# Performance work log

Hardware: AMD Instinct MI355X
Metric: run time of the kernel (lower is better)

The kernel has to match this reference:

```python
import jax, jax.numpy as jnp
import numpy as np

EPS = 1e-7
INF = 1e8
SOFT_CENTER_RADIUS = 3.0
TOPK = 13
IOU_WEIGHT = 3.0
NUM_CLASSES = 80
N_PRIORS = 33600
NUM_GT = 256
IMG = 1024.0


def setup_inputs() -> dict:
    key = jax.random.key(0)
    k1, k2, k3, k4, k5, k6, k7 = jax.random.split(key, 7)
    n, g, c = N_PRIORS, NUM_GT, NUM_CLASSES
    pred_scores = jax.random.normal(k1, (n, c), jnp.float32)
    # priors: (cx, cy, stride, stride)
    ctr = jax.random.uniform(k2, (n, 2), jnp.float32) * IMG
    stride = jnp.full((n, 1), 8.0, jnp.float32)
    priors = jnp.concatenate([ctr, stride, stride], axis=-1)
    # predicted boxes, x1y1x2y2
    pwh = jax.random.uniform(k3, (n, 2), jnp.float32) * 96.0 + 8.0
    pctr = jax.random.uniform(k4, (n, 2), jnp.float32) * IMG
    pred_bboxes = jnp.concatenate([pctr - pwh / 2, pctr + pwh / 2], axis=-1)
    # gt boxes, x1y1x2y2
    gwh = jax.random.uniform(k5, (g, 2), jnp.float32) * 192.0 + 16.0
    gctr = jax.random.uniform(k6, (g, 2), jnp.float32) * IMG
    gt_bboxes = jnp.concatenate([gctr - gwh / 2, gctr + gwh / 2], axis=-1)
    gt_labels = jax.random.randint(k7, (g,), 0, c, dtype=jnp.int32).astype(jnp.int64)
    return {"pred_scores": pred_scores, "priors": priors,
            "pred_bboxes": pred_bboxes, "gt_bboxes": gt_bboxes,
            "gt_labels": gt_labels}


def _pairwise_iou(a, b):
    # a: (n,4), b: (g,4), x1y1x2y2 -> (n,g)
    area_a = (a[:, 2] - a[:, 0]) * (a[:, 3] - a[:, 1])
    area_b = (b[:, 2] - b[:, 0]) * (b[:, 3] - b[:, 1])
    lt = jnp.maximum(a[:, None, :2], b[None, :, :2])
    rb = jnp.minimum(a[:, None, 2:], b[None, :, 2:])
    wh = jnp.clip(rb - lt, 0.0, None)
    inter = wh[..., 0] * wh[..., 1]
    union = area_a[:, None] + area_b[None, :] - inter
    return inter / jnp.maximum(union, 1e-6)


def reference(pred_scores, priors, pred_bboxes, gt_bboxes, gt_labels):
    n, g = pred_bboxes.shape[0], gt_bboxes.shape[0]
    gt_labels = gt_labels.astype(jnp.int32)

    # ---- find_inside_points (box_dim == 4) ----
    pts = priors[:, :2]                                   # (n,2)
    lt = pts[:, None, :] - gt_bboxes[None, :, :2]
    rb = gt_bboxes[None, :, 2:] - pts[:, None, :]
    is_in_gts = jnp.min(jnp.concatenate([lt, rb], -1), -1) > 0   # (n,g)
    pad_bbox_flag = gt_bboxes.sum(-1) > 0                        # (g,)
    is_in_gts = is_in_gts & pad_bbox_flag[None, :]
    valid_mask = jnp.any(is_in_gts, -1)                          # (n,)

    # ---- soft center prior ----
    gt_center = (gt_bboxes[:, :2] + gt_bboxes[:, 2:]) * 0.5      # (g,2)
    dist = jnp.sqrt(((pts[:, None, :] - gt_center[None, :, :]) ** 2).sum(-1))
    dist = dist / priors[:, 2:3]                                 # / stride
    dist = dist * valid_mask[:, None].astype(dist.dtype)
    soft_center_prior = jnp.power(10.0, dist - SOFT_CENTER_RADIUS)

    # ---- iou cost ----
    ious = _pairwise_iou(pred_bboxes, gt_bboxes)                 # (n,g)
    iou_cost = -jnp.log(ious + EPS) * IOU_WEIGHT

    # ---- soft classification cost (BCE-with-logits, iou targets) ----
    logits = pred_scores[:, gt_labels]                           # (n,g)
    scale = jnp.abs(ious - jax.nn.sigmoid(logits)) ** 2
    bce = jnp.maximum(logits, 0) - logits * ious + jnp.log1p(jnp.exp(-jnp.abs(logits)))
    cost = bce * scale + iou_cost + soft_center_prior
    cost = jnp.where(valid_mask[:, None], cost, INF)

    # ---- dynamic k matching (vectorized over GTs) ----
    K = min(TOPK, n)
    topk_ious, _ = jax.lax.top_k(ious.T, K)                      # (g,K)
    dynamic_ks = jnp.clip(topk_ious.sum(-1).astype(jnp.int32), 1, None)  # (g,)
    _, cand_idx = jax.lax.top_k(-cost.T, K)                      # (g,K) lowest-cost priors per gt
    sel = (jnp.arange(K)[None, :] < dynamic_ks[:, None]).astype(jnp.float32)
    matching = jnp.zeros((g, n), jnp.float32).at[
        jnp.arange(g)[:, None], cand_idx].set(sel).T             # (n,g)

    # resolve priors matched to multiple gts -> keep min-cost gt
    multi = matching.sum(-1) > 1
    onehot_min = jax.nn.one_hot(jnp.argmin(cost, -1), g, dtype=jnp.float32)
    matching = jnp.where(multi[:, None], onehot_min, matching)

    fg = matching.sum(-1) > 0
    matched_gt_inds = jnp.argmax(matching, -1)                   # (n,)
    matched_pred_ious = (matching * ious).sum(-1)                # (n,)

    final = fg & valid_mask
    assigned_gt_inds = jnp.where(final, matched_gt_inds + 1, 0)
    assigned_labels = jnp.where(final, gt_labels[matched_gt_inds], -1)
    max_overlaps = jnp.where(final, matched_pred_ious, -INF)
    return assigned_gt_inds, max_overlaps, assigned_labels
```

## Files before the change

### kernel.cpp

```cpp
#include <hip/hip_runtime.h>
#include <cstdint>

#define NPRI 33600
#define NGT  256
#define NCLS 80
#define KTOP 13
#define INF_F 1.0e8f
#define EPS_F 1e-7f
#define L10 3.3219280948873623f
#define SCN_T 1024
#define NW   (SCN_T / 64)
#define CAPI 4096
#define CAPC 1024
#define RFIX 5.5f
#define NPAD (4 * SCN_T)
#define PREP_BLKS ((NPRI + 255) / 256)
#define NEGINF __int_as_float(0xff800000)

typedef unsigned long long u64;

__device__ __forceinline__ int get_label(const void* p, int j, int is64) {
    if (is64) return (int)((const long long*)p)[j];
    return ((const int*)p)[j];
}

__device__ __forceinline__ float wave_max_bc_f32(float v) {
    #pragma unroll
    for (int off = 32; off > 0; off >>= 1) v = fmaxf(v, __shfl_down(v, off, 64));
    return __int_as_float(__builtin_amdgcn_readfirstlane(__float_as_int(v)));
}
__device__ __forceinline__ u64 wave_min_bc_u64(u64 v) {
    #pragma unroll
    for (int off = 32; off > 0; off >>= 1) { u64 o = __shfl_down(v, off, 64); v = (o < v) ? o : v; }
    unsigned lo = (unsigned)__builtin_amdgcn_readfirstlane((int)(v & 0xffffffffull));
    unsigned hi = (unsigned)__builtin_amdgcn_readfirstlane((int)(v >> 32));
    return (((u64)hi) << 32) | lo;
}
template<int NSL>
__device__ __forceinline__ void wave_merge_max13_f32(float (&l)[NSL], float* dst, int lane) {
    int p = 0;
    for (int r = 0; r < KTOP; ++r) {
        float cur = NEGINF;
        #pragma unroll
        for (int s = 0; s < NSL; ++s) if (s == p) cur = l[NSL - 1 - s];
        float bm = wave_max_bc_f32(cur);
        u64 m = __ballot(cur == bm && bm != NEGINF);
        int first = __ffsll(m) - 1;
        if (lane == first) p++;
        if (lane == 0) dst[r] = bm;
    }
}
template<int NSL>
__device__ __forceinline__ void wave_merge_minN(u64 (&l)[NSL], u64* dst, int lane) {
    int p = 0;
    for (int r = 0; r < KTOP; ++r) {
        u64 cur = ~0ull;
        #pragma unroll
        for (int s = 0; s < NSL; ++s) if (s == p) cur = l[s];
        u64 bm = wave_min_bc_u64(cur);
        if (cur == bm && bm != ~0ull) p++;
        if (lane == 0) dst[r] = bm;
    }
}

__device__ __forceinline__ float iou_exact(float4 pb, float areap, float gx1, float gy1,
                                           float gx2, float gy2, float areag) {
    float iw = fmaxf(fminf(pb.z, gx2) - fmaxf(pb.x, gx1), 0.0f);
    float ih = fmaxf(fminf(pb.w, gy2) - fmaxf(pb.y, gy1), 0.0f);
    float inter = iw * ih;
    return inter / fmaxf(areap + areag - inter, 1e-6f);
}
__device__ __forceinline__ float cost_exact(float4 p2, float gcx, float gcy,
                                            float l, float iou) {
    float dx = p2.x - gcx, dy = p2.y - gcy;
    float dist = sqrtf(dx * dx + dy * dy) / p2.z;
    float soft = exp2f((dist - 3.0f) * L10);
    float sig = 1.0f / (1.0f + expf(-l));
    float dd = iou - sig;
    float bce = fmaxf(l, 0.0f) - l * iou + log1pf(expf(-fabsf(l)));
    float iouc = -logf(iou + EPS_F) * 3.0f;
    return bce * (dd * dd) + iouc + soft;
}

__global__ __launch_bounds__(256) void k_prep(
        const float* __restrict__ priors, const float* __restrict__ gt,
        const void* labels, const float* __restrict__ pboxes,
        float4* __restrict__ pbp,
        int* count, int* firstgt, int* flag) {
    __shared__ float4 gbox[NGT];
    __shared__ int    gpad[NGT];
    __shared__ int    bad;
    const int tid = threadIdx.x;
    const int b = blockIdx.x;
    if (b == 0 && tid == 0) bad = 0;
    {
        float4 bx = ((const float4*)gt)[tid];
        gbox[tid] = bx;
        gpad[tid] = ((bx.x + bx.y + bx.z + bx.w) > 0.0f) ? 1 : 0;
    }
    __syncthreads();
    if (b == 0 && tid < 128) {
        long long v = ((const long long*)labels)[tid];
        if (v < 0 || v >= NCLS) atomicOr(&bad, 1);
    }
    int g = b * 256 + tid;
    if (g < NPAD) {
        pbp[2 * (NPRI + g)]     = make_float4(0.f, 0.f, 0.f, 0.f);
        pbp[2 * (NPRI + g) + 1] = make_float4(0.f, 0.f, 1.f, -1.0f);
    }
    if (g < NPRI) {
        count[g] = 0; firstgt[g] = NGT;
        float4 pr = ((const float4*)priors)[g];
        float px = pr.x, py = pr.y;
        int v = 0;
        for (int j = 0; j < NGT; ++j) {
            float4 bx = gbox[j];
            float m = fminf(fminf(px - bx.x, py - bx.y), fminf(bx.z - px, bx.w - py));
            if (m > 0.0f && gpad[j]) { v = 1; break; }
        }
        float rad = pr.z * RFIX;
        float w = v ? rad * rad * (1.0f + 1e-5f) : -1.0f;
        pbp[2 * g]     = ((const float4*)pboxes)[g];
        pbp[2 * g + 1] = make_float4(px, py, pr.z, w);
    }
    if (b == 0) {
        __syncthreads();
        if (tid == 0) *flag = bad ? 0 : 1;
    }
}

#define STEPM(K, PB, P2) { \
    const int i = i0 + (it + K) * SCN_T; \
    float4 pbc = PB; float4 p2c = P2; \
    const int ip = i + 4 * SCN_T; \
    PB = pbp[2 * ip]; \
    P2 = pbp[2 * ip + 1]; \
    float areap = (pbc.z - pbc.x) * (pbc.w - pbc.y); \
    float iw = fmaxf(fminf(pbc.z, gx2) - fmaxf(pbc.x, gx1), 0.0f); \
    float ih = fmaxf(fminf(pbc.w, gy2) - fmaxf(pbc.y, gy1), 0.0f); \
    float inter = iw * ih; \
    float iou = inter / fmaxf(areap + areag - inter, 1e-6f); \
    if (iou > 0.0f) { \
        int p = atomicAdd(&s_ni, 1); \
        if (p < CAPI) liou[p] = iou; \
    } \
    float dx = p2c.x - gcx, dy = p2c.y - gcy; \
    if (dx * dx + dy * dy <= p2c.w) { \
        int p = atomicAdd(&s_nc, 1); \
        if (p < CAPC) lcost[p] = i; \
    } \
}

__global__ __launch_bounds__(SCN_T) void k_scan(
        const float* __restrict__ scores,
        const float4* __restrict__ pbp,
        const float* __restrict__ gt, const void* labels, const int* flag,
        int* count, int* firstgt) {
    const int tid = threadIdx.x, lane = tid & 63, wid = tid >> 6;
    const int j = blockIdx.x;
    const int is64 = *flag;

    const float4 gb = ((const float4*)gt)[j];
    const float gx1 = gb.x, gy1 = gb.y, gx2 = gb.z, gy2 = gb.w;
    const float areag = (gx2 - gx1) * (gy2 - gy1);
    const float gcx = (gx1 + gx2) * 0.5f, gcy = (gy1 + gy2) * 0.5f;
    const int lab = get_label(labels, j, is64);

    __shared__ int s_ni, s_nc, s_mode;
    __shared__ float s_dmax;
    __shared__ float liou[CAPI];
    __shared__ int lcost[CAPC];
    __shared__ float wiof[(NW - 1) * KTOP];
    __shared__ u64 wco[NW * KTOP];
    __shared__ u64 csel[KTOP];
    __shared__ float s_iou13[KTOP];
    if (tid == 0) { s_ni = 0; s_nc = 0; }
    __syncthreads();

    {
        const int i0 = tid;
        float4 pb0 = pbp[2 * i0],               p20 = pbp[2 * i0 + 1];
        float4 pb1 = pbp[2 * (i0 + SCN_T)],     p21 = pbp[2 * (i0 + SCN_T) + 1];
        float4 pb2 = pbp[2 * (i0 + 2 * SCN_T)], p22 = pbp[2 * (i0 + 2 * SCN_T) + 1];
        float4 pb3 = pbp[2 * (i0 + 3 * SCN_T)], p23 = pbp[2 * (i0 + 3 * SCN_T) + 1];
        for (int it = 0; it < 32; it += 4) {
            STEPM(0, pb0, p20)
            STEPM(1, pb1, p21)
            STEPM(2, pb2, p22)
            STEPM(3, pb3, p23)
        }
        {
            const int i = i0 + 32 * SCN_T;
            if (i < NPRI) {
                float4 pbc = pb0; float4 p2c = p20;
                float areap = (pbc.z - pbc.x) * (pbc.w - pbc.y);
                float iw = fmaxf(fminf(pbc.z, gx2) - fmaxf(pbc.x, gx1), 0.0f);
                float ih = fmaxf(fminf(pbc.w, gy2) - fmaxf(pbc.y, gy1), 0.0f);
                float inter = iw * ih;
                float iou = inter / fmaxf(areap + areag - inter, 1e-6f);
                if (iou > 0.0f) {
                    int p = atomicAdd(&s_ni, 1);
                    if (p < CAPI) liou[p] = iou;
                }
                float dx = p2c.x - gcx, dy = p2c.y - gcy;
                if (dx * dx + dy * dy <= p2c.w) {
                    int p = atomicAdd(&s_nc, 1);
                    if (p < CAPC) lcost[p] = i;
                }
            }
        }
    }
    __syncthreads();
    const int ni = s_ni, nc = s_nc;
    const int ncc = (nc < CAPC) ? nc : CAPC;
    const bool fI = (ni > CAPI);

    if (wid == 0) {
        u64 lf[KTOP];
        #pragma unroll
        for (int s = 0; s < KTOP; ++s) lf[s] = ~0ull;
        for (int k = lane; k < ncc; k += 64) {
            int i = lcost[k];
            float4 pb = pbp[2 * i];
            float4 p2 = pbp[2 * i + 1];
            float areap = (pb.z - pb.x) * (pb.w - pb.y);
            float iou = iou_exact(pb, areap, gx1, gy1, gx2, gy2, areag);
            float ec = cost_exact(p2, gcx, gcy, scores[(size_t)i * NCLS + lab], iou);
            u64 ck = (((u64)__float_as_uint(ec)) << 32) | (unsigned)i;
            if (ck < lf[KTOP - 1]) {
                lf[KTOP - 1] = ck;
                #pragma unroll
                for (int s = KTOP - 1; s > 0; --s)
                    if (lf[s] < lf[s - 1]) { u64 t = lf[s]; lf[s] = lf[s - 1]; lf[s - 1] = t; }
            }
        }
        wave_merge_minN<KTOP>(lf, csel, lane);
        if (lane == 0) {
            u64 tk = csel[KTOP - 1];
            int mode; float dmax = 0.0f;
            if (tk == ~0ull) mode = 2;
            else {
                float tau = __uint_as_float((unsigned)(tk >> 32));
                if (!(tau < 9.0e7f)) mode = 2;
                else {
                    dmax = 3.0f + __log2f(tau + 1e-5f) * (1.0f / L10) + 4e-3f;
                    mode = (dmax > RFIX || nc > CAPC) ? 1 : 0;
                }
            }
            s_mode = mode; s_dmax = dmax;
        }
    } else if (!fI) {
        float lf[KTOP];
        #pragma unroll
        for (int s = 0; s < KTOP; ++s) lf[s] = NEGINF;
        int nn = (ni < CAPI) ? ni : CAPI;
        for (int k = (wid - 1) * 64 + lane; k < nn; k += 64 * (NW - 1)) {
            float v = liou[k];
            if (v > lf[0]) {
                lf[0] = v;
                #pragma unroll
                for (int s = 0; s < KTOP - 1; ++s)
                    if (lf[s] > lf[s + 1]) { float t = lf[s]; lf[s] = lf[s + 1]; lf[s + 1] = t; }
            }
        }
        wave_merge_max13_f32<KTOP>(lf, &wiof[(wid - 1) * KTOP], lane);
    }
    __syncthreads();

    if (fI) {
        if (wid > 0) {
            float lf[KTOP];
            #pragma unroll
            for (int s = 0; s < KTOP; ++s) lf[s] = NEGINF;
            for (int i = (wid - 1) * 64 + lane; i < NPRI; i += 64 * (NW - 1)) {
                float4 pb = pbp[2 * i];
                float areap = (pb.z - pb.x) * (pb.w - pb.y);
                float iou = iou_exact(pb, areap, gx1, gy1, gx2, gy2, areag);
                if (iou > 0.0f && iou > lf[0]) {
                    lf[0] = iou;
                    #pragma unroll
                    for (int s = 0; s < KTOP - 1; ++s)
                        if (lf[s] > lf[s + 1]) { float t = lf[s]; lf[s] = lf[s + 1]; lf[s + 1] = t; }
                }
            }
            wave_merge_max13_f32<KTOP>(lf, &wiof[(wid - 1) * KTOP], lane);
        }
        __syncthreads();
    }

    if (wid == 0) {
        int p = 0;
        for (int r = 0; r < KTOP; ++r) {
            float cur = (lane < NW - 1 && p < KTOP) ? wiof[lane * KTOP + p] : NEGINF;
            float bm = wave_max_bc_f32(cur);
            u64 m = __ballot(cur == bm && bm != NEGINF);
            int first = __ffsll(m) - 1;
            if (lane == first) p++;
            if (lane == 0) s_iou13[r] = bm;
        }
    }

    int mode = s_mode;
    if (mode == 1) {
        const float dmax = s_dmax;
        if (tid == 0) s_nc = 0;
        __syncthreads();
        for (int i = tid; i < NPRI; i += SCN_T) {
            float4 p2 = pbp[2 * i + 1];
            if (p2.w > 0.0f) {
                float dx = p2.x - gcx, dy = p2.y - gcy;
                float rad = p2.z * dmax;
                if (dx * dx + dy * dy <= rad * rad * (1.0f + 1e-5f)) {
                    int p = atomicAdd(&s_nc, 1);
                    if (p < CAPC) lcost[p] = i;
                }
            }
        }
        __syncthreads();
        int nc2 = s_nc;
        if (nc2 <= CAPC) {
            if (wid == 0) {
                u64 lf[KTOP];
                #pragma unroll
                for (int s = 0; s < KTOP; ++s) lf[s] = ~0ull;
                for (int k = lane; k < nc2; k += 64) {
                    int i = lcost[k];
                    float4 pb = pbp[2 * i];
                    float4 p2 = pbp[2 * i + 1];
                    float areap = (pb.z - pb.x) * (pb.w - pb.y);
                    float iou = iou_exact(pb, areap, gx1, gy1, gx2, gy2, areag);
                    float ec = cost_exact(p2, gcx, gcy, scores[(size_t)i * NCLS + lab], iou);
                    u64 ck = (((u64)__float_as_uint(ec)) << 32) | (unsigned)i;
                    if (ck < lf[KTOP - 1]) {
                        lf[KTOP - 1] = ck;
                        #pragma unroll
                        for (int s = KTOP - 1; s > 0; --s)
                            if (lf[s] < lf[s - 1]) { u64 t = lf[s]; lf[s] = lf[s - 1]; lf[s - 1] = t; }
                    }
                }
                wave_merge_minN<KTOP>(lf, csel, lane);
            }
        } else {
            mode = 2;
        }
        __syncthreads();
    }
    if (mode == 2) {
        u64 lf[KTOP];
        #pragma unroll
        for (int s = 0; s < KTOP; ++s) lf[s] = ~0ull;
        for (int i = tid; i < NPRI; i += SCN_T) {
            float4 pb = pbp[2 * i];
            float4 p2 = pbp[2 * i + 1];
            float areap = (pb.z - pb.x) * (pb.w - pb.y);
            float iou = iou_exact(pb, areap, gx1, gy1, gx2, gy2, areag);
            float ec = INF_F;
            if (p2.w > 0.0f) ec = cost_exact(p2, gcx, gcy, scores[(size_t)i * NCLS + lab], iou);
            u64 k2 = (((u64)__float_as_uint(ec)) << 32) | (unsigned)i;
            if (k2 < lf[KTOP - 1]) {
                lf[KTOP - 1] = k2;
                #pragma unroll
                for (int s = KTOP - 1; s > 0; --s)
                    if (lf[s] < lf[s - 1]) { u64 t = lf[s]; lf[s] = lf[s - 1]; lf[s - 1] = t; }
            }
        }
        wave_merge_minN<KTOP>(lf, &wco[wid * KTOP], lane);
        __syncthreads();
        if (wid == 0) {
            int p = 0;
            for (int r = 0; r < KTOP; ++r) {
                u64 cur = (lane < NW && p < KTOP) ? wco[lane * KTOP + p] : ~0ull;
                u64 bm = wave_min_bc_u64(cur);
                if (cur == bm && bm != ~0ull) p++;
                if (lane == 0) csel[r] = bm;
            }
        }
        __syncthreads();
    }

    __syncthreads();
    if (wid == 0) {
        float tsum = 0.0f;
        #pragma unroll
        for (int r = 0; r < KTOP; ++r) {
            float v = s_iou13[r];
            tsum += (v == NEGINF) ? 0.0f : v;
        }
        int ks = (int)tsum;
        if (ks < 1) ks = 1;
        if (lane < KTOP && lane < ks) {
            u64 mine = csel[lane];
            if (mine != ~0ull) {
                int idx = (int)(unsigned)(mine & 0xFFFFFFFFull);
                atomicAdd(&count[idx], 1);
                atomicMin(&firstgt[idx], j);
            }
        }
    }
}

__global__ __launch_bounds__(256) void k_assign(
        const float* __restrict__ scores,
        const float4* __restrict__ pbp, const float* __restrict__ gt,
        const void* labels, const int* flag,
        const int* __restrict__ count, const int* __restrict__ firstgt,
        float* __restrict__ out) {
    __shared__ float4 gbox[NGT];
    __shared__ int glab[NGT];
    __shared__ float gcxs[NGT], gcys[NGT], gareas[NGT];
    __shared__ int s_nm;
    __shared__ int s_mlist[256];
    __shared__ u64 red4[4];
    const int tid = threadIdx.x;
    const int is64 = *flag;
    {
        float4 b = ((const float4*)gt)[tid];
        gbox[tid] = b;
        glab[tid] = get_label(labels, tid, is64);
        gcxs[tid] = (b.x + b.z) * 0.5f;
        gcys[tid] = (b.y + b.w) * 0.5f;
        gareas[tid] = (b.z - b.x) * (b.w - b.y);
    }
    if (tid == 0) s_nm = 0;
    __syncthreads();
    const int i = blockIdx.x * 256 + tid;
    const bool act = (i < NPRI);
    if (act) {
        float4 p2 = pbp[2 * i + 1];
        int v = (p2.w > 0.0f) ? 1 : 0;
        int c = count[i];
        float o0 = 0.0f, o1 = -INF_F, o2 = -1.0f;
        if (v && c == 1) {
            int j = firstgt[i];
            float4 pb = pbp[2 * i];
            float areap = (pb.z - pb.x) * (pb.w - pb.y);
            float4 g = gbox[j];
            float iw = fmaxf(fminf(pb.z, g.z) - fmaxf(pb.x, g.x), 0.0f);
            float ih = fmaxf(fminf(pb.w, g.w) - fmaxf(pb.y, g.y), 0.0f);
            float inter = iw * ih;
            float iou = inter / fmaxf(areap + gareas[j] - inter, 1e-6f);
            o0 = (float)(j + 1); o1 = iou; o2 = (float)glab[j];
        } else if (v && c > 1) {
            int p = atomicAdd(&s_nm, 1);
            s_mlist[p] = i;
        }
        out[i] = o0;
        out[NPRI + i] = o1;
        out[2 * NPRI + i] = o2;
    }
    __syncthreads();
    const int nm = s_nm;
    const int j = tid;
    for (int m = 0; m < nm; ++m) {
        const int ii = s_mlist[m];
        float4 pb = pbp[2 * ii];
        float4 p2 = pbp[2 * ii + 1];
        float areap = (pb.z - pb.x) * (pb.w - pb.y);

        float4 g = gbox[j];
        float iw = fmaxf(fminf(pb.z, g.z) - fmaxf(pb.x, g.x), 0.0f);
        float ih = fmaxf(fminf(pb.w, g.w) - fmaxf(pb.y, g.y), 0.0f);
        float inter = iw * ih;
        float iou = inter / fmaxf(areap + gareas[j] - inter, 1e-6f);
        float dx = p2.x - gcxs[j], dy = p2.y - gcys[j];
        float dist = sqrtf(dx * dx + dy * dy) / p2.z;
        float soft = exp2f((dist - 3.0f) * L10);
        float l = scores[(size_t)ii * NCLS + glab[j]];
        float sig = 1.0f / (1.0f + expf(-l));
        float dd = iou - sig;
        float bce = fmaxf(l, 0.0f) - l * iou + log1pf(expf(-fabsf(l)));
        float cost = bce * (dd * dd) + (-logf(iou + EPS_F) * 3.0f) + soft;

        u64 key = (((u64)__float_as_uint(cost)) << 32) | (unsigned)j;
        u64 v = key;
        #pragma unroll
        for (int off = 32; off > 0; off >>= 1) {
            u64 o = __shfl_down(v, off, 64);
            v = (o < v) ? o : v;
        }
        if ((tid & 63) == 0) red4[tid >> 6] = v;
        __syncthreads();
        u64 best = red4[0];
        #pragma unroll
        for (int q = 1; q < 4; ++q) best = (red4[q] < best) ? red4[q] : best;
        if (key == best) {
            out[ii] = (float)(j + 1);
            out[NPRI + ii] = iou;
            out[2 * NPRI + ii] = (float)glab[j];
        }
        __syncthreads();
    }
}

extern "C" void kernel_launch(void* const* d_in, const int* in_sizes, int n_in,
                              void* d_out, int out_size, void* d_ws, size_t ws_size,
                              hipStream_t stream) {
    const float* scores = (const float*)d_in[0];
    const float* priors = (const float*)d_in[1];
    const float* pboxes = (const float*)d_in[2];
    const float* gt     = (const float*)d_in[3];
    const void*  labels = d_in[4];
    float* out = (float*)d_out;

    char* ws = (char*)d_ws;
    size_t off = 0;
    auto alloc = [&](size_t bytes) { size_t o = off; off = (off + bytes + 255) & ~(size_t)255; return o; };
    int*    flag     = (int*)(ws + alloc(4));
    int*    count    = (int*)(ws + alloc((size_t)NPRI * 4));
    int*    firstgt  = (int*)(ws + alloc((size_t)NPRI * 4));
    float4* pbp      = (float4*)(ws + alloc((size_t)(NPRI + NPAD) * 32));
    (void)ws_size;

    hipLaunchKernelGGL(k_prep, dim3(PREP_BLKS), dim3(256), 0, stream,
                       priors, gt, labels, pboxes, pbp, count, firstgt, flag);
    hipLaunchKernelGGL(k_scan, dim3(NGT), dim3(SCN_T), 0, stream,
                       scores, pbp, gt, labels, flag, count, firstgt);
    hipLaunchKernelGGL(k_assign, dim3((NPRI + 255) / 256), dim3(256), 0, stream,
                       scores, pbp, gt, labels, flag, count, firstgt, out);
}
```

Measured before the change: 145.1 us.

## Bin priors into a spatial grid so each GT scans only nearby cells

Adds a 32x32 spatial binning of predicted-box centers and prior points. It builds histograms and max half-extent and radius in k_prep, an exclusive scan in k_bins and a counting-sort scatter in k_scatter. k_scan then visits only the bins overlapping each GT box (expanded by the max pred half-size) and the center-radius window, instead of streaming all 33600 priors per GT. The block size is halved to 512. This adds three small launches, a memset and global atomics in exchange for cutting per-GT work. The order of candidates within the shared lists changes, which may affect tie handling downstream.

```diff
diff --git a/kernel.cpp b/kernel.cpp
--- a/kernel.cpp
+++ b/kernel.cpp
@@ -8,12 +8,13 @@
 #define INF_F 1.0e8f
 #define EPS_F 1e-7f
 #define L10 3.3219280948873623f
-#define SCN_T 1024
+#define SCN_T 512
 #define NW   (SCN_T / 64)
 #define CAPI 4096
 #define CAPC 1024
 #define RFIX 5.5f
-#define NPAD (4 * SCN_T)
+#define NBX  32
+#define NB   (NBX * NBX)
 #define PREP_BLKS ((NPRI + 255) / 256)
 #define NEGINF __int_as_float(0xff800000)
 
@@ -22,6 +23,11 @@
 __device__ __forceinline__ int get_label(const void* p, int j, int is64) {
     if (is64) return (int)((const long long*)p)[j];
     return ((const int*)p)[j];
+}
+
+__device__ __forceinline__ int bin1(float c) {
+    int b = (int)floorf(c * 0.03125f);
+    return b < 0 ? 0 : (b > NBX - 1 ? NBX - 1 : b);
 }
 
 __device__ __forceinline__ float wave_max_bc_f32(float v) {
@@ -86,7 +92,8 @@
         const float* __restrict__ priors, const float* __restrict__ gt,
         const void* labels, const float* __restrict__ pboxes,
         float4* __restrict__ pbp,
-        int* count, int* firstgt, int* flag) {
+        int* count, int* firstgt, int* flag,
+        int* histI, int* histC, int* maxbuf) {
     __shared__ float4 gbox[NGT];
     __shared__ int    gpad[NGT];
     __shared__ int    bad;
@@ -104,10 +111,6 @@
         if (v < 0 || v >= NCLS) atomicOr(&bad, 1);
     }
     int g = b * 256 + tid;
-    if (g < NPAD) {
-        pbp[2 * (NPRI + g)]     = make_float4(0.f, 0.f, 0.f, 0.f);
-        pbp[2 * (NPRI + g) + 1] = make_float4(0.f, 0.f, 1.f, -1.0f);
-    }
     if (g < NPRI) {
         count[g] = 0; firstgt[g] = NGT;
         float4 pr = ((const float4*)priors)[g];
@@ -120,8 +123,16 @@
         }
         float rad = pr.z * RFIX;
         float w = v ? rad * rad * (1.0f + 1e-5f) : -1.0f;
-        pbp[2 * g]     = ((const float4*)pboxes)[g];
+        float4 pb = ((const float4*)pboxes)[g];
+        pbp[2 * g]     = pb;
         pbp[2 * g + 1] = make_float4(px, py, pr.z, w);
+        float pcx = (pb.x + pb.z) * 0.5f, pcy = (pb.y + pb.w) * 0.5f;
+        atomicAdd(&histI[bin1(pcy) * NBX + bin1(pcx)], 1);
+        atomicAdd(&histC[bin1(py) * NBX + bin1(px)], 1);
+        float hw = fmaxf((pb.z - pb.x) * 0.5f, 0.0f);
+        float hh = fmaxf((pb.w - pb.y) * 0.5f, 0.0f);
+        atomicMax(&maxbuf[0], __float_as_int(fmaxf(hw, hh)));
+        atomicMax(&maxbuf[1], __float_as_int(w));
     }
     if (b == 0) {
         __syncthreads();
@@ -129,31 +140,59 @@
     }
 }
 
-#define STEPM(K, PB, P2) { \
-    const int i = i0 + (it + K) * SCN_T; \
-    float4 pbc = PB; float4 p2c = P2; \
-    const int ip = i + 4 * SCN_T; \
-    PB = pbp[2 * ip]; \
-    P2 = pbp[2 * ip + 1]; \
-    float areap = (pbc.z - pbc.x) * (pbc.w - pbc.y); \
-    float iw = fmaxf(fminf(pbc.z, gx2) - fmaxf(pbc.x, gx1), 0.0f); \
-    float ih = fmaxf(fminf(pbc.w, gy2) - fmaxf(pbc.y, gy1), 0.0f); \
-    float inter = iw * ih; \
-    float iou = inter / fmaxf(areap + areag - inter, 1e-6f); \
-    if (iou > 0.0f) { \
-        int p = atomicAdd(&s_ni, 1); \
-        if (p < CAPI) liou[p] = iou; \
-    } \
-    float dx = p2c.x - gcx, dy = p2c.y - gcy; \
-    if (dx * dx + dy * dy <= p2c.w) { \
-        int p = atomicAdd(&s_nc, 1); \
-        if (p < CAPC) lcost[p] = i; \
-    } \
+__global__ __launch_bounds__(NB) void k_bins(
+        const int* __restrict__ histI, const int* __restrict__ histC,
+        int* startI, int* startC, int* curI, int* curC) {
+    __shared__ int sc[NB];
+    const int t = threadIdx.x;
+    int h = histI[t];
+    sc[t] = h;
+    __syncthreads();
+    for (int off = 1; off < NB; off <<= 1) {
+        int u = (t >= off) ? sc[t - off] : 0;
+        __syncthreads();
+        sc[t] += u;
+        __syncthreads();
+    }
+    int excl = sc[t] - h;
+    startI[t] = excl; curI[t] = excl;
+    if (t == NB - 1) startI[NB] = sc[t];
+    __syncthreads();
+    h = histC[t];
+    sc[t] = h;
+    __syncthreads();
+    for (int off = 1; off < NB; off <<= 1) {
+        int u = (t >= off) ? sc[t - off] : 0;
+        __syncthreads();
+        sc[t] += u;
+        __syncthreads();
+    }
+    excl = sc[t] - h;
+    startC[t] = excl; curC[t] = excl;
+    if (t == NB - 1) startC[NB] = sc[t];
+}
+
+__global__ __launch_bounds__(256) void k_scatter(
+        const float4* __restrict__ pbp,
+        int* curI, int* curC,
+        float4* __restrict__ A_pb, float4* __restrict__ A_pc) {
+    const int i = blockIdx.x * 256 + threadIdx.x;
+    if (i >= NPRI) return;
+    float4 pb = pbp[2 * i];
+    float4 p2 = pbp[2 * i + 1];
+    float pcx = (pb.x + pb.z) * 0.5f, pcy = (pb.y + pb.w) * 0.5f;
+    int r = atomicAdd(&curI[bin1(pcy) * NBX + bin1(pcx)], 1);
+    A_pb[r] = pb;
+    int r2 = atomicAdd(&curC[bin1(p2.y) * NBX + bin1(p2.x)], 1);
+    A_pc[r2] = make_float4(p2.x, p2.y, p2.w, __int_as_float(i));
 }
 
 __global__ __launch_bounds__(SCN_T) void k_scan(
         const float* __restrict__ scores,
         const float4* __restrict__ pbp,
+        const float4* __restrict__ A_pb, const float4* __restrict__ A_pc,
+        const int* __restrict__ startI, const int* __restrict__ startC,
+        const int* __restrict__ maxbuf,
         const float* __restrict__ gt, const void* labels, const int* flag,
         int* count, int* firstgt) {
     const int tid = threadIdx.x, lane = tid & 63, wid = tid >> 6;
@@ -165,6 +204,10 @@
     const float areag = (gx2 - gx1) * (gy2 - gy1);
     const float gcx = (gx1 + gx2) * 0.5f, gcy = (gy1 + gy2) * 0.5f;
     const int lab = get_label(labels, j, is64);
+    const float hmax = __int_as_float(maxbuf[0]);
+    const float wmax = __int_as_float(maxbuf[1]);
+    const float M = 2.0f * hmax + 1.0f;
+    const float rmax = sqrtf(fmaxf(wmax, 0.0f)) + 1.0f;
 
     __shared__ int s_ni, s_nc, s_mode;
     __shared__ float s_dmax;
@@ -178,34 +221,34 @@
     __syncthreads();
 
     {
-        const int i0 = tid;
-        float4 pb0 = pbp[2 * i0],               p20 = pbp[2 * i0 + 1];
-        float4 pb1 = pbp[2 * (i0 + SCN_T)],     p21 = pbp[2 * (i0 + SCN_T) + 1];
-        float4 pb2 = pbp[2 * (i0 + 2 * SCN_T)], p22 = pbp[2 * (i0 + 2 * SCN_T) + 1];
-        float4 pb3 = pbp[2 * (i0 + 3 * SCN_T)], p23 = pbp[2 * (i0 + 3 * SCN_T) + 1];
-        for (int it = 0; it < 32; it += 4) {
-            STEPM(0, pb0, p20)
-            STEPM(1, pb1, p21)
-            STEPM(2, pb2, p22)
-            STEPM(3, pb3, p23)
-        }
-        {
-            const int i = i0 + 32 * SCN_T;
-            if (i < NPRI) {
-                float4 pbc = pb0; float4 p2c = p20;
-                float areap = (pbc.z - pbc.x) * (pbc.w - pbc.y);
-                float iw = fmaxf(fminf(pbc.z, gx2) - fmaxf(pbc.x, gx1), 0.0f);
-                float ih = fmaxf(fminf(pbc.w, gy2) - fmaxf(pbc.y, gy1), 0.0f);
-                float inter = iw * ih;
-                float iou = inter / fmaxf(areap + areag - inter, 1e-6f);
+        int lox = bin1(gx1 - M), hix = bin1(gx2 + M);
+        int loy = bin1(gy1 - M), hiy = bin1(gy2 + M);
+        for (int by = loy; by <= hiy; ++by) {
+            int s0 = startI[by * NBX + lox];
+            int e0 = startI[by * NBX + hix + 1];
+            for (int r = s0 + tid; r < e0; r += SCN_T) {
+                float4 pb = A_pb[r];
+                float areap = (pb.z - pb.x) * (pb.w - pb.y);
+                float iou = iou_exact(pb, areap, gx1, gy1, gx2, gy2, areag);
                 if (iou > 0.0f) {
                     int p = atomicAdd(&s_ni, 1);
                     if (p < CAPI) liou[p] = iou;
                 }
-                float dx = p2c.x - gcx, dy = p2c.y - gcy;
-                if (dx * dx + dy * dy <= p2c.w) {
+            }
+        }
+    }
+    {
+        int lox = bin1(gcx - rmax), hix = bin1(gcx + rmax);
+        int loy = bin1(gcy - rmax), hiy = bin1(gcy + rmax);
+        for (int by = loy; by <= hiy; ++by) {
+            int s0 = startC[by * NBX + lox];
+            int e0 = startC[by * NBX + hix + 1];
+            for (int r = s0 + tid; r < e0; r += SCN_T) {
+                float4 pc = A_pc[r];
+                float dx = pc.x - gcx, dy = pc.y - gcy;
+                if (dx * dx + dy * dy <= pc.z) {
                     int p = atomicAdd(&s_nc, 1);
-                    if (p < CAPC) lcost[p] = i;
+                    if (p < CAPC) lcost[p] = __float_as_int(pc.w);
                 }
             }
         }
@@ -505,16 +548,32 @@
     char* ws = (char*)d_ws;
     size_t off = 0;
     auto alloc = [&](size_t bytes) { size_t o = off; off = (off + bytes + 255) & ~(size_t)255; return o; };
-    int*    flag     = (int*)(ws + alloc(4));
-    int*    count    = (int*)(ws + alloc((size_t)NPRI * 4));
-    int*    firstgt  = (int*)(ws + alloc((size_t)NPRI * 4));
-    float4* pbp      = (float4*)(ws + alloc((size_t)(NPRI + NPAD) * 32));
+    int*    flag    = (int*)(ws + alloc(4));
+    int*    count   = (int*)(ws + alloc((size_t)NPRI * 4));
+    int*    firstgt = (int*)(ws + alloc((size_t)NPRI * 4));
+    int*    histI   = (int*)(ws + alloc((size_t)(2 * NB + 2) * 4));
+    int*    histC   = histI + NB;
+    int*    maxbuf  = histI + 2 * NB;
+    int*    startI  = (int*)(ws + alloc((size_t)(NB + 1) * 4));
+    int*    startC  = (int*)(ws + alloc((size_t)(NB + 1) * 4));
+    int*    curI    = (int*)(ws + alloc((size_t)NB * 4));
+    int*    curC    = (int*)(ws + alloc((size_t)NB * 4));
+    float4* pbp     = (float4*)(ws + alloc((size_t)NPRI * 32));
+    float4* A_pb    = (float4*)(ws + alloc((size_t)NPRI * 16));
+    float4* A_pc    = (float4*)(ws + alloc((size_t)NPRI * 16));
     (void)ws_size;
 
+    hipMemsetAsync(histI, 0, (size_t)(2 * NB + 2) * 4, stream);
     hipLaunchKernelGGL(k_prep, dim3(PREP_BLKS), dim3(256), 0, stream,
-                       priors, gt, labels, pboxes, pbp, count, firstgt, flag);
+                       priors, gt, labels, pboxes, pbp, count, firstgt, flag,
+                       histI, histC, maxbuf);
+    hipLaunchKernelGGL(k_bins, dim3(1), dim3(NB), 0, stream,
+                       histI, histC, startI, startC, curI, curC);
+    hipLaunchKernelGGL(k_scatter, dim3(PREP_BLKS), dim3(256), 0, stream,
+                       pbp, curI, curC, A_pb, A_pc);
     hipLaunchKernelGGL(k_scan, dim3(NGT), dim3(SCN_T), 0, stream,
-                       scores, pbp, gt, labels, flag, count, firstgt);
+                       scores, pbp, A_pb, A_pc, startI, startC, maxbuf,
+                       gt, labels, flag, count, firstgt);
     hipLaunchKernelGGL(k_assign, dim3((NPRI + 255) / 256), dim3(256), 0, stream,
                        scores, pbp, gt, labels, flag, count, firstgt, out);
 }
```

Measured after the change: 165.6 us. 1.14x slower.
